# Performance work log

Hardware: AMD Instinct MI355X
Metric: run time of the kernel (lower is better)

## Reference

```python
import jax, jax.numpy as jnp
import numpy as np

N, D, E = 50000, 64, 800000  # nodes, node_dim, edges


def setup_inputs() -> dict:
    key = jax.random.key(0)
    ks = jax.random.split(key, 9)
    def lin(kw, fan_in, fan_out):
        # torch nn.Linear default init: U(-1/sqrt(fan_in), 1/sqrt(fan_in))
        bound = 1.0 / np.sqrt(fan_in)
        kw1, kw2 = jax.random.split(kw)
        W = jax.random.uniform(kw1, (fan_in, fan_out), jnp.float32, -bound, bound)
        b = jax.random.uniform(kw2, (fan_out,), jnp.float32, -bound, bound)
        return W, b
    W1, b1 = lin(ks[0], 2 * D + 2, D)
    W2, b2 = lin(ks[1], D, D // 2)
    W3, b3 = lin(ks[2], D // 2, D // 4)
    return {
        "node_features": jax.random.normal(ks[3], (N, D), jnp.float32),
        "edge_index": jax.random.randint(ks[4], (2, E), 0, N, jnp.int64),
        "spatial_features": jax.random.normal(ks[5], (E, 2), jnp.float32),
        "W1": W1, "b1": b1, "W2": W2, "b2": b2, "W3": W3, "b3": b3,
    }


def reference(node_features, edge_index, spatial_features, W1, b1, W2, b2, W3, b3):
    src = node_features[edge_index[0]]          # [E, D] gather
    dst = node_features[edge_index[1]]          # [E, D] gather
    x = jnp.concatenate([src, dst, spatial_features], axis=1)  # [E, 2D+2]
    h = jax.nn.relu(x @ W1 + b1)                # [E, D]
    h = jax.nn.relu(h @ W2 + b2)                # [E, D//2]
    return h @ W3 + b3                          # [E, D//4]
```

## Files before the change

kernel.cpp:

```cpp
#include <hip/hip_runtime.h>
#include <hip/hip_bf16.h>

#define NE 800000
#define NN 50000
#define TPW 4
#define NTILES (NE / 16)
#define NODE_TILES (NN / 16)
#define W1LD 136

typedef __attribute__((ext_vector_type(8))) short        s16x8;
typedef __attribute__((ext_vector_type(8))) __bf16       bf16x8;
typedef __attribute__((ext_vector_type(4))) float        f32x4;
typedef __attribute__((ext_vector_type(2))) float        f32x2;
typedef __attribute__((ext_vector_type(4))) unsigned int u32x4;
typedef __attribute__((ext_vector_type(2))) unsigned int u32x2;

#define TAB_OFF 16384
#define WS_TAB ((size_t)(TAB_OFF + 2ull * NN * 64) * 2)
#define WS_NFB ((size_t)(TAB_OFF + 1ull * NN * 64) * 2)

__device__ __forceinline__ unsigned short f2bf_bits(float f) {
    __bf16 b = (__bf16)f;
    return __builtin_bit_cast(unsigned short, b);
}

__device__ __forceinline__ unsigned int pkbf(float a, float b) {
    return (unsigned int)f2bf_bits(a) | ((unsigned int)f2bf_bits(b) << 16);
}

__device__ __forceinline__ s16x8 cvt8(f32x4 a, f32x4 b) {
    bf16x8 r;
    r[0] = (__bf16)a[0]; r[1] = (__bf16)a[1]; r[2] = (__bf16)a[2]; r[3] = (__bf16)a[3];
    r[4] = (__bf16)b[0]; r[5] = (__bf16)b[1]; r[6] = (__bf16)b[2]; r[7] = (__bf16)b[3];
    return __builtin_bit_cast(s16x8, r);
}

__global__ __launch_bounds__(256) void node_prep_all(
    const float* __restrict__ nf, const float* __restrict__ W1,
    const float* __restrict__ b1, const float* __restrict__ W2,
    const float* __restrict__ W3, unsigned short* __restrict__ ws) {
    unsigned short* w2t = ws + 10240;
    unsigned short* w3t = ws + 12288;
    unsigned short* At  = ws + TAB_OFF;
    unsigned short* Bt  = At + (size_t)NN * 64;

    __shared__ unsigned short w1l[64 * W1LD];

    const int tid = threadIdx.x, wid = tid >> 6, lane = tid & 63;
    const int lr = lane & 15, lg = lane >> 4;

    for (int i = tid; i < 128 * 64; i += 256) {
        const int k = i >> 6, j = i & 63;
        w1l[j * W1LD + k] = f2bf_bits(W1[i]);
    }
    __syncthreads();

    if (blockIdx.x == 0) {
        for (int i = tid; i < 32 * 64; i += 256) {
            int j = i / 64, k = i % 64;
            w2t[i] = f2bf_bits(W2[k * 32 + j]);
        }
        for (int i = tid; i < 16 * 32; i += 256) {
            int j = i / 32, k = i % 32;
            w3t[i] = f2bf_bits(W3[k * 16 + j]);
        }
    }

    s16x8 w1f[4][4];
    #pragma unroll
    for (int s = 0; s < 4; ++s)
        #pragma unroll
        for (int c = 0; c < 4; ++c)
            w1f[s][c] = *reinterpret_cast<const s16x8*>(
                &w1l[(c * 16 + lr) * W1LD + s * 32 + lg * 8]);

    f32x4 b1q[4];
    #pragma unroll
    for (int c = 0; c < 4; ++c)
        b1q[c] = *reinterpret_cast<const f32x4*>(b1 + c * 16 + lg * 4);

    const int tile = blockIdx.x * 4 + wid;
    if (tile >= NODE_TILES) return;

    const int row = tile * 16 + lr;
    const float* p = nf + (long)row * 64;
    s16x8 nfr[2];
    #pragma unroll
    for (int s = 0; s < 2; ++s) {
        f32x4 a = *reinterpret_cast<const f32x4*>(p + s * 32 + lg * 8);
        f32x4 b = *reinterpret_cast<const f32x4*>(p + s * 32 + lg * 8 + 4);
        nfr[s] = cvt8(a, b);
    }
    f32x4 a4[4], b4[4];
    #pragma unroll
    for (int c = 0; c < 4; ++c) { a4[c] = (f32x4){0,0,0,0}; b4[c] = (f32x4){0,0,0,0}; }
    #pragma unroll
    for (int s = 0; s < 2; ++s)
        #pragma unroll
        for (int c = 0; c < 4; ++c) {
            a4[c] = __builtin_amdgcn_mfma_f32_16x16x32_bf16(w1f[s][c],     nfr[s], a4[c], 0, 0, 0);
            b4[c] = __builtin_amdgcn_mfma_f32_16x16x32_bf16(w1f[s + 2][c], nfr[s], b4[c], 0, 0, 0);
        }
    #pragma unroll
    for (int c = 0; c < 4; ++c) {
        u32x2 pa, pb;
        pa[0] = pkbf(a4[c][0] + b1q[c][0], a4[c][1] + b1q[c][1]);
        pa[1] = pkbf(a4[c][2] + b1q[c][2], a4[c][3] + b1q[c][3]);
        pb[0] = pkbf(b4[c][0], b4[c][1]);
        pb[1] = pkbf(b4[c][2], b4[c][3]);
        *reinterpret_cast<u32x2*>(At + (long)row * 64 + c * 16 + lg * 4) = pa;
        *reinterpret_cast<u32x2*>(Bt + (long)row * 64 + c * 16 + lg * 4) = pb;
    }
}

__device__ __forceinline__ void gatherT(const unsigned short* At, const unsigned short* Bt,
                                        int si, int di, int lg, s16x8 g[4]) {
    const unsigned short* pa = At + (size_t)si * 64 + lg * 8;
    const unsigned short* pb = Bt + (size_t)di * 64 + lg * 8;
    g[0] = *reinterpret_cast<const s16x8*>(pa);
    g[1] = *reinterpret_cast<const s16x8*>(pa + 32);
    g[2] = *reinterpret_cast<const s16x8*>(pb);
    g[3] = *reinterpret_cast<const s16x8*>(pb + 32);
}

__device__ __forceinline__ void compute_tile(
    int tile, const s16x8 cur[4], f32x2 s2,
    const f32x2 c0p[2][4], const f32x2 c1p[2][4],
    const s16x8 w2f[2][2], s16x8 w3f,
    const f32x4 b2v[2], f32x4 b3v,
    unsigned short* h2w, int lg, int lr, float* __restrict__ out) {

    const f32x2 sp0v = {s2[0], s2[0]}, sp1v = {s2[1], s2[1]};

    s16x8 bfr[2];
    #pragma unroll
    for (int jb = 0; jb < 2; ++jb) {
        u32x4 au = __builtin_bit_cast(u32x4, cur[jb]);
        u32x4 bu = __builtin_bit_cast(u32x4, cur[2 + jb]);
        u32x4 pk4;
        #pragma unroll
        for (int q = 0; q < 4; ++q) {
            f32x2 av = {__builtin_bit_cast(float, au[q] << 16),
                        __builtin_bit_cast(float, au[q] & 0xFFFF0000u)};
            f32x2 bv = {__builtin_bit_cast(float, bu[q] << 16),
                        __builtin_bit_cast(float, bu[q] & 0xFFFF0000u)};
            f32x2 h = av + bv;
            h = sp1v * c1p[jb][q] + h;
            h = sp0v * c0p[jb][q] + h;
            pk4[q] = pkbf(fmaxf(h[0], 0.f), fmaxf(h[1], 0.f));
        }
        bfr[jb] = __builtin_bit_cast(s16x8, pk4);
    }

    f32x4 acc2[2];
    #pragma unroll
    for (int c = 0; c < 2; ++c) acc2[c] = (f32x4){0, 0, 0, 0};
    #pragma unroll
    for (int s = 0; s < 2; ++s)
        #pragma unroll
        for (int c = 0; c < 2; ++c)
            acc2[c] = __builtin_amdgcn_mfma_f32_16x16x32_bf16(w2f[s][c], bfr[s], acc2[c], 0, 0, 0);

    #pragma unroll
    for (int c = 0; c < 2; ++c) {
        u32x2 p;
        p[0] = pkbf(fmaxf(acc2[c][0] + b2v[c][0], 0.f), fmaxf(acc2[c][1] + b2v[c][1], 0.f));
        p[1] = pkbf(fmaxf(acc2[c][2] + b2v[c][2], 0.f), fmaxf(acc2[c][3] + b2v[c][3], 0.f));
        *reinterpret_cast<u32x2*>(h2w + c * 16 + lg * 4) = p;
    }

    s16x8 bf3 = *reinterpret_cast<const s16x8*>(h2w + lg * 8);
    f32x4 acc3 = (f32x4){0, 0, 0, 0};
    acc3 = __builtin_amdgcn_mfma_f32_16x16x32_bf16(w3f, bf3, acc3, 0, 0, 0);

    f32x4 o;
    #pragma unroll
    for (int r = 0; r < 4; ++r) o[r] = acc3[r] + b3v[r];
    __builtin_nontemporal_store(o,
        reinterpret_cast<f32x4*>(out + (long)(tile * 16 + lr) * 16 + lg * 4));
}

__global__ __launch_bounds__(256) void edge_mlp_tab(
    const int* __restrict__ ei, const float* __restrict__ sp,
    const float* __restrict__ W1, const float* __restrict__ b2,
    const float* __restrict__ b3, const unsigned short* __restrict__ wsw,
    float* __restrict__ out) {

    const unsigned short* w2t = wsw + 10240;
    const unsigned short* w3t = wsw + 12288;
    const unsigned short* At  = wsw + TAB_OFF;
    const unsigned short* Bt  = At + (size_t)NN * 64;

    __shared__ unsigned short h2s[4 * 16 * 40];

    const int tid = threadIdx.x, wid = tid >> 6, lane = tid & 63;
    const int lr = lane & 15, lg = lane >> 4;

    const int tile0 = (blockIdx.x * 4 + wid) * TPW;

    s16x8 w2f[2][2], w3f;
    #pragma unroll
    for (int s = 0; s < 2; ++s)
        #pragma unroll
        for (int c = 0; c < 2; ++c)
            w2f[s][c] = *reinterpret_cast<const s16x8*>(w2t + (c * 16 + lr) * 64 + s * 32 + lg * 8);
    w3f = *reinterpret_cast<const s16x8*>(w3t + lr * 32 + lg * 8);

    f32x4 b2v[2];
    #pragma unroll
    for (int c = 0; c < 2; ++c) b2v[c] = *reinterpret_cast<const f32x4*>(b2 + c * 16 + lg * 4);
    const f32x4 b3v = *reinterpret_cast<const f32x4*>(b3 + lg * 4);

    f32x2 c0p[2][4], c1p[2][4];
    #pragma unroll
    for (int jb = 0; jb < 2; ++jb) {
        const int j0 = jb * 32 + lg * 8;
        f32x4 x0 = *reinterpret_cast<const f32x4*>(W1 + 128 * 64 + j0);
        f32x4 x1 = *reinterpret_cast<const f32x4*>(W1 + 128 * 64 + j0 + 4);
        f32x4 y0 = *reinterpret_cast<const f32x4*>(W1 + 129 * 64 + j0);
        f32x4 y1 = *reinterpret_cast<const f32x4*>(W1 + 129 * 64 + j0 + 4);
        c0p[jb][0] = (f32x2){x0[0], x0[1]}; c0p[jb][1] = (f32x2){x0[2], x0[3]};
        c0p[jb][2] = (f32x2){x1[0], x1[1]}; c0p[jb][3] = (f32x2){x1[2], x1[3]};
        c1p[jb][0] = (f32x2){y0[0], y0[1]}; c1p[jb][1] = (f32x2){y0[2], y0[3]};
        c1p[jb][2] = (f32x2){y1[0], y1[1]}; c1p[jb][3] = (f32x2){y1[2], y1[3]};
    }

    unsigned short* h2w = h2s + wid * (16 * 40) + lr * 40;

    int si[TPW], di[TPW];
    f32x2 spv[TPW];
    #pragma unroll
    for (int t = 0; t < TPW; ++t) {
        const size_t e = (size_t)(tile0 + t) * 16 + lr;
        si[t] = ei[e];
        di[t] = ei[NE + e];
        spv[t] = *reinterpret_cast<const f32x2*>(sp + 2 * e);
    }

    s16x8 cur[4], nxt[4];
    gatherT(At, Bt, si[0], di[0], lg, cur);

    #pragma unroll
    for (int tt = 0; tt < TPW; ++tt) {
        if (tt + 1 < TPW)
            gatherT(At, Bt, si[tt + 1], di[tt + 1], lg, nxt);
        compute_tile(tile0 + tt, cur, spv[tt], c0p, c1p, w2f, w3f,
                     b2v, b3v, h2w, lg, lr, out);
        #pragma unroll
        for (int s = 0; s < 4; ++s) cur[s] = nxt[s];
    }
}

__global__ void prep(const float* __restrict__ W1, const float* __restrict__ W2,
                     const float* __restrict__ W3, const float* __restrict__ nf,
                     unsigned short* __restrict__ ws, int do_nf) {
    unsigned short* w1t = ws;
    unsigned short* w2t = ws + 10240;
    unsigned short* w3t = ws + 12288;
    int t = blockIdx.x * blockDim.x + threadIdx.x;
    int stride = gridDim.x * blockDim.x;
    for (int i = t; i < 64 * 160; i += stride) {
        int j = i / 160, k = i % 160;
        w1t[i] = f2bf_bits(k < 130 ? W1[k * 64 + j] : 0.0f);
    }
    for (int i = t; i < 32 * 64; i += stride) {
        int j = i / 64, k = i % 64;
        w2t[i] = f2bf_bits(W2[k * 32 + j]);
    }
    for (int i = t; i < 16 * 32; i += stride) {
        int j = i / 32, k = i % 32;
        w3t[i] = f2bf_bits(W3[k * 16 + j]);
    }
    if (do_nf) {
        unsigned short* nfb = ws + TAB_OFF;
        for (int i = t; i < NN * 8; i += stride) {
            f32x4 a = *reinterpret_cast<const f32x4*>(nf + (long)i * 8);
            f32x4 b = *reinterpret_cast<const f32x4*>(nf + (long)i * 8 + 4);
            *reinterpret_cast<s16x8*>(nfb + (long)i * 8) = cvt8(a, b);
        }
    }
}

template <bool BF16NF>
__device__ __forceinline__ void gather4(const unsigned short* nfb, const float* nf,
                                        int si, int di, int lg, s16x8 g[4]) {
    if (BF16NF) {
        #pragma unroll
        for (int s = 0; s < 4; ++s) {
            const int row = (s < 2) ? si : di;
            g[s] = *reinterpret_cast<const s16x8*>(nfb + (long)row * 64 + (s & 1) * 32 + lg * 8);
        }
    } else {
        #pragma unroll
        for (int s = 0; s < 4; ++s) {
            const float* p = nf + (long)((s < 2) ? si : di) * 64 + (s & 1) * 32 + lg * 8;
            f32x4 a = *reinterpret_cast<const f32x4*>(p);
            f32x4 b = *reinterpret_cast<const f32x4*>(p + 4);
            g[s] = cvt8(a, b);
        }
    }
}

template <bool BF16NF>
__global__ __launch_bounds__(256) void edge_mlp_fb(
    const float* __restrict__ nf, const int* __restrict__ ei,
    const float* __restrict__ sp, const float* __restrict__ b1,
    const float* __restrict__ b2, const float* __restrict__ b3,
    const unsigned short* __restrict__ wsw, float* __restrict__ out) {

    const unsigned short* w1t = wsw;
    const unsigned short* w2t = wsw + 10240;
    const unsigned short* w3t = wsw + 12288;
    const unsigned short* nfb = wsw + TAB_OFF;

    __shared__ float h1s[4][16][68];
    __shared__ float h2s[4][16][36];

    const int tid = threadIdx.x, wid = tid >> 6, lane = tid & 63;
    const int lr = lane & 15, lg = lane >> 4;

    s16x8 w1f[5][4], w2f[2][2], w3f;
    #pragma unroll
    for (int s = 0; s < 5; ++s)
        #pragma unroll
        for (int c = 0; c < 4; ++c)
            w1f[s][c] = *reinterpret_cast<const s16x8*>(w1t + (c * 16 + lr) * 160 + s * 32 + lg * 8);
    #pragma unroll
    for (int s = 0; s < 2; ++s)
        #pragma unroll
        for (int c = 0; c < 2; ++c)
            w2f[s][c] = *reinterpret_cast<const s16x8*>(w2t + (c * 16 + lr) * 64 + s * 32 + lg * 8);
    w3f = *reinterpret_cast<const s16x8*>(w3t + lr * 32 + lg * 8);

    float bias1[4], bias2[2], bias3;
    #pragma unroll
    for (int c = 0; c < 4; ++c) bias1[c] = b1[c * 16 + lr];
    #pragma unroll
    for (int c = 0; c < 2; ++c) bias2[c] = b2[c * 16 + lr];
    bias3 = b3[lr];

    const int tile0 = (blockIdx.x * 4 + wid) * 4;
    int si[4], di[4];
    f32x2 spv[4];
    #pragma unroll
    for (int t = 0; t < 4; ++t) {
        const int e = (tile0 + t) * 16 + lr;
        si[t] = ei[e];
        di[t] = ei[NE + e];
        spv[t] = *reinterpret_cast<const f32x2*>(sp + 2 * (size_t)e);
    }

    s16x8 cur[4], nxt[4];
    gather4<BF16NF>(nfb, nf, si[0], di[0], lg, cur);

    #pragma unroll
    for (int tt = 0; tt < 4; ++tt) {
        if (tt + 1 < 4)
            gather4<BF16NF>(nfb, nf, si[tt + 1], di[tt + 1], lg, nxt);

        const int ebase = (tile0 + tt) * 16;

        f32x4 acc1[4];
        #pragma unroll
        for (int c = 0; c < 4; ++c) acc1[c] = (f32x4){0, 0, 0, 0};
        #pragma unroll
        for (int s = 0; s < 4; ++s)
            #pragma unroll
            for (int c = 0; c < 4; ++c)
                acc1[c] = __builtin_amdgcn_mfma_f32_16x16x32_bf16(cur[s], w1f[s][c], acc1[c], 0, 0, 0);
        {
            bf16x8 z;
            #pragma unroll
            for (int j = 0; j < 8; ++j) z[j] = (__bf16)0.0f;
            if (lg == 0) { z[0] = (__bf16)spv[tt][0]; z[1] = (__bf16)spv[tt][1]; }
            s16x8 af = __builtin_bit_cast(s16x8, z);
            #pragma unroll
            for (int c = 0; c < 4; ++c)
                acc1[c] = __builtin_amdgcn_mfma_f32_16x16x32_bf16(af, w1f[4][c], acc1[c], 0, 0, 0);
        }
        #pragma unroll
        for (int c = 0; c < 4; ++c)
            #pragma unroll
            for (int r = 0; r < 4; ++r)
                h1s[wid][lg * 4 + r][c * 16 + lr] = fmaxf(acc1[c][r] + bias1[c], 0.0f);

        f32x4 acc2[2];
        #pragma unroll
        for (int c = 0; c < 2; ++c) acc2[c] = (f32x4){0, 0, 0, 0};
        #pragma unroll
        for (int s = 0; s < 2; ++s) {
            f32x4 a = *reinterpret_cast<const f32x4*>(&h1s[wid][lr][s * 32 + lg * 8]);
            f32x4 b = *reinterpret_cast<const f32x4*>(&h1s[wid][lr][s * 32 + lg * 8 + 4]);
            s16x8 af = cvt8(a, b);
            #pragma unroll
            for (int c = 0; c < 2; ++c)
                acc2[c] = __builtin_amdgcn_mfma_f32_16x16x32_bf16(af, w2f[s][c], acc2[c], 0, 0, 0);
        }
        #pragma unroll
        for (int c = 0; c < 2; ++c)
            #pragma unroll
            for (int r = 0; r < 4; ++r)
                h2s[wid][lg * 4 + r][c * 16 + lr] = fmaxf(acc2[c][r] + bias2[c], 0.0f);

        f32x4 a3 = *reinterpret_cast<const f32x4*>(&h2s[wid][lr][lg * 8]);
        f32x4 b3x = *reinterpret_cast<const f32x4*>(&h2s[wid][lr][lg * 8 + 4]);
        s16x8 af3 = cvt8(a3, b3x);
        f32x4 acc3 = (f32x4){0, 0, 0, 0};
        acc3 = __builtin_amdgcn_mfma_f32_16x16x32_bf16(af3, w3f, acc3, 0, 0, 0);
        #pragma unroll
        for (int r = 0; r < 4; ++r)
            out[(long)(ebase + lg * 4 + r) * 16 + lr] = acc3[r] + bias3;

        #pragma unroll
        for (int s = 0; s < 4; ++s) cur[s] = nxt[s];
    }
}

extern "C" void kernel_launch(void* const* d_in, const int* in_sizes, int n_in,
                              void* d_out, int out_size, void* d_ws, size_t ws_size,
                              hipStream_t stream) {
    const float* nf = (const float*)d_in[0];
    const int*   ei = (const int*)d_in[1];
    const float* sp = (const float*)d_in[2];
    const float* W1 = (const float*)d_in[3];
    const float* b1 = (const float*)d_in[4];
    const float* W2 = (const float*)d_in[5];
    const float* b2 = (const float*)d_in[6];
    const float* W3 = (const float*)d_in[7];
    const float* b3 = (const float*)d_in[8];
    float* out = (float*)d_out;
    unsigned short* wsw = (unsigned short*)d_ws;

    const bool tab  = (ws_size >= WS_TAB);
    const bool bnfb = (!tab && ws_size >= WS_NFB);

    if (tab) {
        const int pblocks = (NODE_TILES + 3) / 4;
        hipLaunchKernelGGL(node_prep_all, dim3(pblocks), dim3(256), 0, stream,
                           nf, W1, b1, W2, W3, wsw);
        const int blocks = NTILES / TPW / 4;
        hipLaunchKernelGGL(edge_mlp_tab, dim3(blocks), dim3(256), 0, stream,
                           ei, sp, W1, b2, b3, wsw, out);
    } else {
        hipLaunchKernelGGL(prep, dim3(64), dim3(256), 0, stream,
                           W1, W2, W3, nf, wsw, bnfb ? 1 : 0);
        const int blocks = NTILES / 4 / 4;
        if (bnfb)
            hipLaunchKernelGGL(edge_mlp_fb<true>, dim3(blocks), dim3(256), 0, stream,
                               nf, ei, sp, b1, b2, b3, wsw, out);
        else
            hipLaunchKernelGGL(edge_mlp_fb<false>, dim3(blocks), dim3(256), 0, stream,
                               nf, ei, sp, b1, b2, b3, wsw, out);
    }
}
```

Measured before the change: 60.23 us.

## Split W1 packing into single-block kernel and halve edge tiles per wave

Moves the bf16 conversion and fragment packing of W1, W2 and W3 out of the per-block node prep kernel into a separate one-block kernel that writes MFMA-ready fragments to workspace. Each node_prep block then loads its W1 fragments directly from global memory, so the 782 blocks no longer each convert and transpose the whole W1 through shared memory. TPW also drops from 4 to 2, doubling the edge kernel's grid for more parallelism. The cost is an extra kernel launch plus serialization behind a single-block kernel.

```diff
diff --git a/kernel.cpp b/kernel.cpp
--- a/kernel.cpp
+++ b/kernel.cpp
@@ -3,10 +3,9 @@
 
 #define NE 800000
 #define NN 50000
-#define TPW 4
+#define TPW 2
 #define NTILES (NE / 16)
 #define NODE_TILES (NN / 16)
-#define W1LD 136
 
 typedef __attribute__((ext_vector_type(8))) short        s16x8;
 typedef __attribute__((ext_vector_type(8))) __bf16       bf16x8;
@@ -35,44 +34,45 @@
     return __builtin_bit_cast(s16x8, r);
 }
 
-__global__ __launch_bounds__(256) void node_prep_all(
-    const float* __restrict__ nf, const float* __restrict__ W1,
-    const float* __restrict__ b1, const float* __restrict__ W2,
+__global__ __launch_bounds__(256) void pack_weights_tab(
+    const float* __restrict__ W1, const float* __restrict__ W2,
     const float* __restrict__ W3, unsigned short* __restrict__ ws) {
+    __shared__ unsigned short w1l[128 * 64];
+    const int tid = threadIdx.x;
+    for (int i = tid; i < 128 * 64; i += 256) w1l[i] = f2bf_bits(W1[i]);
+    __syncthreads();
+    for (int i = tid; i < 8192; i += 256) {
+        const int b = i & 7, idx = i >> 3;
+        const int f = idx & 15, lane = idx >> 4;
+        const int s = f >> 2, c = f & 3, lr = lane & 15, lg = lane >> 4;
+        ws[i] = w1l[(s * 32 + lg * 8 + b) * 64 + c * 16 + lr];
+    }
     unsigned short* w2t = ws + 10240;
     unsigned short* w3t = ws + 12288;
-    unsigned short* At  = ws + TAB_OFF;
-    unsigned short* Bt  = At + (size_t)NN * 64;
-
-    __shared__ unsigned short w1l[64 * W1LD];
-
+    for (int i = tid; i < 32 * 64; i += 256) {
+        int j = i / 64, k = i % 64;
+        w2t[i] = f2bf_bits(W2[k * 32 + j]);
+    }
+    for (int i = tid; i < 16 * 32; i += 256) {
+        int j = i / 32, k = i % 32;
+        w3t[i] = f2bf_bits(W3[k * 16 + j]);
+    }
+}
+
+__global__ __launch_bounds__(256) void node_prep(
+    const float* __restrict__ nf, const float* __restrict__ b1,
+    const unsigned short* __restrict__ wsw, unsigned short* __restrict__ At,
+    unsigned short* __restrict__ Bt) {
     const int tid = threadIdx.x, wid = tid >> 6, lane = tid & 63;
     const int lr = lane & 15, lg = lane >> 4;
 
-    for (int i = tid; i < 128 * 64; i += 256) {
-        const int k = i >> 6, j = i & 63;
-        w1l[j * W1LD + k] = f2bf_bits(W1[i]);
-    }
-    __syncthreads();
-
-    if (blockIdx.x == 0) {
-        for (int i = tid; i < 32 * 64; i += 256) {
-            int j = i / 64, k = i % 64;
-            w2t[i] = f2bf_bits(W2[k * 32 + j]);
-        }
-        for (int i = tid; i < 16 * 32; i += 256) {
-            int j = i / 32, k = i % 32;
-            w3t[i] = f2bf_bits(W3[k * 16 + j]);
-        }
-    }
-
     s16x8 w1f[4][4];
     #pragma unroll
     for (int s = 0; s < 4; ++s)
         #pragma unroll
         for (int c = 0; c < 4; ++c)
             w1f[s][c] = *reinterpret_cast<const s16x8*>(
-                &w1l[(c * 16 + lr) * W1LD + s * 32 + lg * 8]);
+                wsw + ((size_t)lane * 16 + s * 4 + c) * 8);
 
     f32x4 b1q[4];
     #pragma unroll
@@ -435,9 +435,11 @@
     const bool bnfb = (!tab && ws_size >= WS_NFB);
 
     if (tab) {
+        hipLaunchKernelGGL(pack_weights_tab, dim3(1), dim3(256), 0, stream,
+                           W1, W2, W3, wsw);
         const int pblocks = (NODE_TILES + 3) / 4;
-        hipLaunchKernelGGL(node_prep_all, dim3(pblocks), dim3(256), 0, stream,
-                           nf, W1, b1, W2, W3, wsw);
+        hipLaunchKernelGGL(node_prep, dim3(pblocks), dim3(256), 0, stream,
+                           nf, b1, wsw, wsw + TAB_OFF, wsw + TAB_OFF + (size_t)NN * 64);
         const int blocks = NTILES / TPW / 4;
         hipLaunchKernelGGL(edge_mlp_tab, dim3(blocks), dim3(256), 0, stream,
                            ei, sp, W1, b2, b3, wsw, out);
```

Result: slower. 78.44 us (+30.2%).

## Fuse node prep and edge MLP into one persistent cooperative kernel

Applied to the files above, without the earlier changes.

Replaces the two-launch path (node table precompute, then edge MLP) with a single persistent cooperative kernel. Its waves first build the per-node W1 projection tables, then pass a grid-wide sync and loop over edge tile pairs while prefetching the next indices. This removes one kernel launch and the gap between kernels. In exchange it adds a grid barrier, host-side occupancy queries on every call, and weight fragments built from strided global reads. If the cooperative launch fails, it falls back to the old two-kernel path.

```diff
diff --git a/kernel.cpp b/kernel.cpp
--- a/kernel.cpp
+++ b/kernel.cpp
@@ -1,11 +1,15 @@
 #include <hip/hip_runtime.h>
 #include <hip/hip_bf16.h>
+#include <hip/hip_cooperative_groups.h>
+
+namespace cg = cooperative_groups;
 
 #define NE 800000
 #define NN 50000
 #define TPW 4
 #define NTILES (NE / 16)
 #define NODE_TILES (NN / 16)
+#define NUNITS (NTILES / 2)
 #define W1LD 136
 
 typedef __attribute__((ext_vector_type(8))) short        s16x8;
@@ -33,84 +37,6 @@
     r[0] = (__bf16)a[0]; r[1] = (__bf16)a[1]; r[2] = (__bf16)a[2]; r[3] = (__bf16)a[3];
     r[4] = (__bf16)b[0]; r[5] = (__bf16)b[1]; r[6] = (__bf16)b[2]; r[7] = (__bf16)b[3];
     return __builtin_bit_cast(s16x8, r);
-}
-
-__global__ __launch_bounds__(256) void node_prep_all(
-    const float* __restrict__ nf, const float* __restrict__ W1,
-    const float* __restrict__ b1, const float* __restrict__ W2,
-    const float* __restrict__ W3, unsigned short* __restrict__ ws) {
-    unsigned short* w2t = ws + 10240;
-    unsigned short* w3t = ws + 12288;
-    unsigned short* At  = ws + TAB_OFF;
-    unsigned short* Bt  = At + (size_t)NN * 64;
-
-    __shared__ unsigned short w1l[64 * W1LD];
-
-    const int tid = threadIdx.x, wid = tid >> 6, lane = tid & 63;
-    const int lr = lane & 15, lg = lane >> 4;
-
-    for (int i = tid; i < 128 * 64; i += 256) {
-        const int k = i >> 6, j = i & 63;
-        w1l[j * W1LD + k] = f2bf_bits(W1[i]);
-    }
-    __syncthreads();
-
-    if (blockIdx.x == 0) {
-        for (int i = tid; i < 32 * 64; i += 256) {
-            int j = i / 64, k = i % 64;
-            w2t[i] = f2bf_bits(W2[k * 32 + j]);
-        }
-        for (int i = tid; i < 16 * 32; i += 256) {
-            int j = i / 32, k = i % 32;
-            w3t[i] = f2bf_bits(W3[k * 16 + j]);
-        }
-    }
-
-    s16x8 w1f[4][4];
-    #pragma unroll
-    for (int s = 0; s < 4; ++s)
-        #pragma unroll
-        for (int c = 0; c < 4; ++c)
-            w1f[s][c] = *reinterpret_cast<const s16x8*>(
-                &w1l[(c * 16 + lr) * W1LD + s * 32 + lg * 8]);
-
-    f32x4 b1q[4];
-    #pragma unroll
-    for (int c = 0; c < 4; ++c)
-        b1q[c] = *reinterpret_cast<const f32x4*>(b1 + c * 16 + lg * 4);
-
-    const int tile = blockIdx.x * 4 + wid;
-    if (tile >= NODE_TILES) return;
-
-    const int row = tile * 16 + lr;
-    const float* p = nf + (long)row * 64;
-    s16x8 nfr[2];
-    #pragma unroll
-    for (int s = 0; s < 2; ++s) {
-        f32x4 a = *reinterpret_cast<const f32x4*>(p + s * 32 + lg * 8);
-        f32x4 b = *reinterpret_cast<const f32x4*>(p + s * 32 + lg * 8 + 4);
-        nfr[s] = cvt8(a, b);
-    }
-    f32x4 a4[4], b4[4];
-    #pragma unroll
-    for (int c = 0; c < 4; ++c) { a4[c] = (f32x4){0,0,0,0}; b4[c] = (f32x4){0,0,0,0}; }
-    #pragma unroll
-    for (int s = 0; s < 2; ++s)
-        #pragma unroll
-        for (int c = 0; c < 4; ++c) {
-            a4[c] = __builtin_amdgcn_mfma_f32_16x16x32_bf16(w1f[s][c],     nfr[s], a4[c], 0, 0, 0);
-            b4[c] = __builtin_amdgcn_mfma_f32_16x16x32_bf16(w1f[s + 2][c], nfr[s], b4[c], 0, 0, 0);
-        }
-    #pragma unroll
-    for (int c = 0; c < 4; ++c) {
-        u32x2 pa, pb;
-        pa[0] = pkbf(a4[c][0] + b1q[c][0], a4[c][1] + b1q[c][1]);
-        pa[1] = pkbf(a4[c][2] + b1q[c][2], a4[c][3] + b1q[c][3]);
-        pb[0] = pkbf(b4[c][0], b4[c][1]);
-        pb[1] = pkbf(b4[c][2], b4[c][3]);
-        *reinterpret_cast<u32x2*>(At + (long)row * 64 + c * 16 + lg * 4) = pa;
-        *reinterpret_cast<u32x2*>(Bt + (long)row * 64 + c * 16 + lg * 4) = pb;
-    }
 }
 
 __device__ __forceinline__ void gatherT(const unsigned short* At, const unsigned short* Bt,
@@ -178,6 +104,231 @@
     for (int r = 0; r < 4; ++r) o[r] = acc3[r] + b3v[r];
     __builtin_nontemporal_store(o,
         reinterpret_cast<f32x4*>(out + (long)(tile * 16 + lr) * 16 + lg * 4));
+}
+
+__device__ __forceinline__ void load_unit_idx(const int* __restrict__ ei,
+                                              const float* __restrict__ sp, int u, int lr,
+                                              int si[2], int di[2], f32x2 spv[2]) {
+    #pragma unroll
+    for (int v = 0; v < 2; ++v) {
+        const size_t e = (size_t)(u * 2 + v) * 16 + lr;
+        si[v] = ei[e];
+        di[v] = ei[NE + e];
+        spv[v] = *reinterpret_cast<const f32x2*>(sp + 2 * e);
+    }
+}
+
+__global__ __launch_bounds__(256, 4) void fused_all(
+    const float* __restrict__ nf, const int* __restrict__ ei,
+    const float* __restrict__ sp, const float* __restrict__ W1,
+    const float* __restrict__ b1, const float* __restrict__ W2,
+    const float* __restrict__ b2, const float* __restrict__ W3,
+    const float* __restrict__ b3, unsigned short* __restrict__ tab,
+    float* __restrict__ out) {
+
+    unsigned short* At = tab;
+    unsigned short* Bt = tab + (size_t)NN * 64;
+
+    __shared__ unsigned short h2s[4 * 16 * 40];
+
+    const int tid = threadIdx.x, wid = tid >> 6, lane = tid & 63;
+    const int lr = lane & 15, lg = lane >> 4;
+    const int gwave  = blockIdx.x * 4 + wid;
+    const int nwaves = gridDim.x * 4;
+
+    if (gwave < NODE_TILES) {
+        s16x8 w1f[4][4];
+        #pragma unroll
+        for (int s = 0; s < 4; ++s)
+            #pragma unroll
+            for (int c = 0; c < 4; ++c) {
+                bf16x8 w;
+                #pragma unroll
+                for (int b = 0; b < 8; ++b)
+                    w[b] = (__bf16)W1[(s * 32 + lg * 8 + b) * 64 + c * 16 + lr];
+                w1f[s][c] = __builtin_bit_cast(s16x8, w);
+            }
+        f32x4 b1q[4];
+        #pragma unroll
+        for (int c = 0; c < 4; ++c)
+            b1q[c] = *reinterpret_cast<const f32x4*>(b1 + c * 16 + lg * 4);
+
+        for (int tile = gwave; tile < NODE_TILES; tile += nwaves) {
+            const int row = tile * 16 + lr;
+            const float* p = nf + (long)row * 64;
+            s16x8 nfr[2];
+            #pragma unroll
+            for (int s = 0; s < 2; ++s) {
+                f32x4 a = *reinterpret_cast<const f32x4*>(p + s * 32 + lg * 8);
+                f32x4 b = *reinterpret_cast<const f32x4*>(p + s * 32 + lg * 8 + 4);
+                nfr[s] = cvt8(a, b);
+            }
+            f32x4 a4[4], b4[4];
+            #pragma unroll
+            for (int c = 0; c < 4; ++c) { a4[c] = (f32x4){0,0,0,0}; b4[c] = (f32x4){0,0,0,0}; }
+            #pragma unroll
+            for (int s = 0; s < 2; ++s)
+                #pragma unroll
+                for (int c = 0; c < 4; ++c) {
+                    a4[c] = __builtin_amdgcn_mfma_f32_16x16x32_bf16(w1f[s][c],     nfr[s], a4[c], 0, 0, 0);
+                    b4[c] = __builtin_amdgcn_mfma_f32_16x16x32_bf16(w1f[s + 2][c], nfr[s], b4[c], 0, 0, 0);
+                }
+            #pragma unroll
+            for (int c = 0; c < 4; ++c) {
+                u32x2 pa, pb;
+                pa[0] = pkbf(a4[c][0] + b1q[c][0], a4[c][1] + b1q[c][1]);
+                pa[1] = pkbf(a4[c][2] + b1q[c][2], a4[c][3] + b1q[c][3]);
+                pb[0] = pkbf(b4[c][0], b4[c][1]);
+                pb[1] = pkbf(b4[c][2], b4[c][3]);
+                *reinterpret_cast<u32x2*>(At + (long)row * 64 + c * 16 + lg * 4) = pa;
+                *reinterpret_cast<u32x2*>(Bt + (long)row * 64 + c * 16 + lg * 4) = pb;
+            }
+        }
+    }
+
+    __threadfence();
+    cg::this_grid().sync();
+
+    s16x8 w2f[2][2];
+    #pragma unroll
+    for (int s = 0; s < 2; ++s)
+        #pragma unroll
+        for (int c = 0; c < 2; ++c) {
+            bf16x8 w;
+            #pragma unroll
+            for (int b = 0; b < 8; ++b)
+                w[b] = (__bf16)W2[(s * 32 + lg * 8 + b) * 32 + c * 16 + lr];
+            w2f[s][c] = __builtin_bit_cast(s16x8, w);
+        }
+    s16x8 w3f;
+    {
+        bf16x8 w;
+        #pragma unroll
+        for (int b = 0; b < 8; ++b) w[b] = (__bf16)W3[(lg * 8 + b) * 16 + lr];
+        w3f = __builtin_bit_cast(s16x8, w);
+    }
+
+    f32x4 b2v[2];
+    #pragma unroll
+    for (int c = 0; c < 2; ++c) b2v[c] = *reinterpret_cast<const f32x4*>(b2 + c * 16 + lg * 4);
+    const f32x4 b3v = *reinterpret_cast<const f32x4*>(b3 + lg * 4);
+
+    f32x2 c0p[2][4], c1p[2][4];
+    #pragma unroll
+    for (int jb = 0; jb < 2; ++jb) {
+        const int j0 = jb * 32 + lg * 8;
+        f32x4 x0 = *reinterpret_cast<const f32x4*>(W1 + 128 * 64 + j0);
+        f32x4 x1 = *reinterpret_cast<const f32x4*>(W1 + 128 * 64 + j0 + 4);
+        f32x4 y0 = *reinterpret_cast<const f32x4*>(W1 + 129 * 64 + j0);
+        f32x4 y1 = *reinterpret_cast<const f32x4*>(W1 + 129 * 64 + j0 + 4);
+        c0p[jb][0] = (f32x2){x0[0], x0[1]}; c0p[jb][1] = (f32x2){x0[2], x0[3]};
+        c0p[jb][2] = (f32x2){x1[0], x1[1]}; c0p[jb][3] = (f32x2){x1[2], x1[3]};
+        c1p[jb][0] = (f32x2){y0[0], y0[1]}; c1p[jb][1] = (f32x2){y0[2], y0[3]};
+        c1p[jb][2] = (f32x2){y1[0], y1[1]}; c1p[jb][3] = (f32x2){y1[2], y1[3]};
+    }
+
+    unsigned short* h2w = h2s + wid * (16 * 40) + lr * 40;
+
+    int u = gwave;
+    if (u < NUNITS) {
+        int si[2], di[2];
+        f32x2 spv[2];
+        load_unit_idx(ei, sp, u, lr, si, di, spv);
+        for (;;) {
+            const int un = u + nwaves;
+            const bool more = (un < NUNITS);
+            s16x8 cur[4], nxt[4];
+            gatherT(At, Bt, si[0], di[0], lg, cur);
+            int si2[2], di2[2];
+            f32x2 spv2[2];
+            if (more) load_unit_idx(ei, sp, un, lr, si2, di2, spv2);
+            gatherT(At, Bt, si[1], di[1], lg, nxt);
+            compute_tile(u * 2,     cur, spv[0], c0p, c1p, w2f, w3f, b2v, b3v, h2w, lg, lr, out);
+            compute_tile(u * 2 + 1, nxt, spv[1], c0p, c1p, w2f, w3f, b2v, b3v, h2w, lg, lr, out);
+            if (!more) break;
+            #pragma unroll
+            for (int v = 0; v < 2; ++v) { si[v] = si2[v]; di[v] = di2[v]; spv[v] = spv2[v]; }
+            u = un;
+        }
+    }
+}
+
+__global__ __launch_bounds__(256) void node_prep_all(
+    const float* __restrict__ nf, const float* __restrict__ W1,
+    const float* __restrict__ b1, const float* __restrict__ W2,
+    const float* __restrict__ W3, unsigned short* __restrict__ ws) {
+    unsigned short* w2t = ws + 10240;
+    unsigned short* w3t = ws + 12288;
+    unsigned short* At  = ws + TAB_OFF;
+    unsigned short* Bt  = At + (size_t)NN * 64;
+
+    __shared__ unsigned short w1l[64 * W1LD];
+
+    const int tid = threadIdx.x, wid = tid >> 6, lane = tid & 63;
+    const int lr = lane & 15, lg = lane >> 4;
+
+    for (int i = tid; i < 128 * 64; i += 256) {
+        const int k = i >> 6, j = i & 63;
+        w1l[j * W1LD + k] = f2bf_bits(W1[i]);
+    }
+    __syncthreads();
+
+    if (blockIdx.x == 0) {
+        for (int i = tid; i < 32 * 64; i += 256) {
+            int j = i / 64, k = i % 64;
+            w2t[i] = f2bf_bits(W2[k * 32 + j]);
+        }
+        for (int i = tid; i < 16 * 32; i += 256) {
+            int j = i / 32, k = i % 32;
+            w3t[i] = f2bf_bits(W3[k * 16 + j]);
+        }
+    }
+
+    s16x8 w1f[4][4];
+    #pragma unroll
+    for (int s = 0; s < 4; ++s)
+        #pragma unroll
+        for (int c = 0; c < 4; ++c)
+            w1f[s][c] = *reinterpret_cast<const s16x8*>(
+                &w1l[(c * 16 + lr) * W1LD + s * 32 + lg * 8]);
+
+    f32x4 b1q[4];
+    #pragma unroll
+    for (int c = 0; c < 4; ++c)
+        b1q[c] = *reinterpret_cast<const f32x4*>(b1 + c * 16 + lg * 4);
+
+    const int tile = blockIdx.x * 4 + wid;
+    if (tile >= NODE_TILES) return;
+
+    const int row = tile * 16 + lr;
+    const float* p = nf + (long)row * 64;
+    s16x8 nfr[2];
+    #pragma unroll
+    for (int s = 0; s < 2; ++s) {
+        f32x4 a = *reinterpret_cast<const f32x4*>(p + s * 32 + lg * 8);
+        f32x4 b = *reinterpret_cast<const f32x4*>(p + s * 32 + lg * 8 + 4);
+        nfr[s] = cvt8(a, b);
+    }
+    f32x4 a4[4], b4[4];
+    #pragma unroll
+    for (int c = 0; c < 4; ++c) { a4[c] = (f32x4){0,0,0,0}; b4[c] = (f32x4){0,0,0,0}; }
+    #pragma unroll
+    for (int s = 0; s < 2; ++s)
+        #pragma unroll
+        for (int c = 0; c < 4; ++c) {
+            a4[c] = __builtin_amdgcn_mfma_f32_16x16x32_bf16(w1f[s][c],     nfr[s], a4[c], 0, 0, 0);
+            b4[c] = __builtin_amdgcn_mfma_f32_16x16x32_bf16(w1f[s + 2][c], nfr[s], b4[c], 0, 0, 0);
+        }
+    #pragma unroll
+    for (int c = 0; c < 4; ++c) {
+        u32x2 pa, pb;
+        pa[0] = pkbf(a4[c][0] + b1q[c][0], a4[c][1] + b1q[c][1]);
+        pa[1] = pkbf(a4[c][2] + b1q[c][2], a4[c][3] + b1q[c][3]);
+        pb[0] = pkbf(b4[c][0], b4[c][1]);
+        pb[1] = pkbf(b4[c][2], b4[c][3]);
+        *reinterpret_cast<u32x2*>(At + (long)row * 64 + c * 16 + lg * 4) = pa;
+        *reinterpret_cast<u32x2*>(Bt + (long)row * 64 + c * 16 + lg * 4) = pb;
+    }
 }
 
 __global__ __launch_bounds__(256) void edge_mlp_tab(
@@ -435,12 +586,30 @@
     const bool bnfb = (!tab && ws_size >= WS_NFB);
 
     if (tab) {
-        const int pblocks = (NODE_TILES + 3) / 4;
-        hipLaunchKernelGGL(node_prep_all, dim3(pblocks), dim3(256), 0, stream,
-                           nf, W1, b1, W2, W3, wsw);
-        const int blocks = NTILES / TPW / 4;
-        hipLaunchKernelGGL(edge_mlp_tab, dim3(blocks), dim3(256), 0, stream,
-                           ei, sp, W1, b2, b3, wsw, out);
+        bool done = false;
+        int maxb = 0, ncu = 0;
+        if (hipOccupancyMaxActiveBlocksPerMultiprocessor(
+                &maxb, (const void*)fused_all, 256, 0) == hipSuccess &&
+            hipDeviceGetAttribute(&ncu, hipDeviceAttributeMultiprocessorCount, 0)
+                == hipSuccess && maxb > 0 && ncu > 0) {
+            int grid = maxb * ncu;
+            if (grid > 2048) grid = 2048;
+            unsigned short* tabp = wsw + TAB_OFF;
+            void* args[] = {(void*)&nf, (void*)&ei, (void*)&sp, (void*)&W1,
+                            (void*)&b1, (void*)&W2, (void*)&b2, (void*)&W3,
+                            (void*)&b3, (void*)&tabp, (void*)&out};
+            hipError_t le = hipLaunchCooperativeKernel(
+                (const void*)fused_all, dim3(grid), dim3(256), args, 0, stream);
+            done = (le == hipSuccess);
+        }
+        if (!done) {
+            const int pblocks = (NODE_TILES + 3) / 4;
+            hipLaunchKernelGGL(node_prep_all, dim3(pblocks), dim3(256), 0, stream,
+                               nf, W1, b1, W2, W3, wsw);
+            const int blocks = NTILES / TPW / 4;
+            hipLaunchKernelGGL(edge_mlp_tab, dim3(blocks), dim3(256), 0, stream,
+                               ei, sp, W1, b2, b3, wsw, out);
+        }
     } else {
         hipLaunchKernelGGL(prep, dim3(64), dim3(256), 0, stream,
                            W1, W2, W3, nf, wsw, bnfb ? 1 : 0);
```

After: 179.0 us. +197.1%, slower.

## Deepen gather prefetch to two tiles ahead and swizzle W1 LDS layout

Applied to the files above, without the earlier changes.

Each wave in the edge kernel now processes five tiles instead of four. It keeps three gather buffers so table gathers run two tiles ahead of compute, aiming to hide more of the latency of random node-table reads. The node-prep kernel now loads W1 with float4 vector loads and stores it into LDS with an XOR swizzle, meant to reduce bank conflicts on both the write and the fragment reads. The costs are higher register pressure from the extra buffer and fewer, larger blocks. NTILES/(TPW*4) divides evenly at 2500 blocks, so no edges are dropped.

```diff
diff --git a/kernel.cpp b/kernel.cpp
--- a/kernel.cpp
+++ b/kernel.cpp
@@ -3,13 +3,15 @@
 
 #define NE 800000
 #define NN 50000
-#define TPW 4
+#define TPW 5
 #define NTILES (NE / 16)
 #define NODE_TILES (NN / 16)
-#define W1LD 136
+#define W1STR 136
 
 typedef __attribute__((ext_vector_type(8))) short        s16x8;
+typedef __attribute__((ext_vector_type(4))) short        s16x4;
 typedef __attribute__((ext_vector_type(8))) __bf16       bf16x8;
+typedef __attribute__((ext_vector_type(4))) __bf16       bf16x4;
 typedef __attribute__((ext_vector_type(4))) float        f32x4;
 typedef __attribute__((ext_vector_type(2))) float        f32x2;
 typedef __attribute__((ext_vector_type(4))) unsigned int u32x4;
@@ -33,6 +35,10 @@
     r[0] = (__bf16)a[0]; r[1] = (__bf16)a[1]; r[2] = (__bf16)a[2]; r[3] = (__bf16)a[3];
     r[4] = (__bf16)b[0]; r[5] = (__bf16)b[1]; r[6] = (__bf16)b[2]; r[7] = (__bf16)b[3];
     return __builtin_bit_cast(s16x8, r);
+}
+
+__device__ __forceinline__ int w1addr(int k, int j) {
+    return j * W1STR + (((k >> 3) ^ ((j >> 2) & 15)) << 3) + (k & 7);
 }
 
 __global__ __launch_bounds__(256) void node_prep_all(
@@ -44,14 +50,19 @@
     unsigned short* At  = ws + TAB_OFF;
     unsigned short* Bt  = At + (size_t)NN * 64;
 
-    __shared__ unsigned short w1l[64 * W1LD];
+    __shared__ unsigned short w1l[64 * W1STR];
 
     const int tid = threadIdx.x, wid = tid >> 6, lane = tid & 63;
     const int lr = lane & 15, lg = lane >> 4;
 
-    for (int i = tid; i < 128 * 64; i += 256) {
-        const int k = i >> 6, j = i & 63;
-        w1l[j * W1LD + k] = f2bf_bits(W1[i]);
+    #pragma unroll
+    for (int it = 0; it < 8; ++it) {
+        const int i = it * 1024 + tid * 4;
+        const int k = i >> 6, j0 = i & 63;
+        f32x4 v = *reinterpret_cast<const f32x4*>(W1 + i);
+        #pragma unroll
+        for (int q = 0; q < 4; ++q)
+            w1l[w1addr(k, j0 + q)] = f2bf_bits(v[q]);
     }
     __syncthreads();
 
@@ -72,7 +83,7 @@
         #pragma unroll
         for (int c = 0; c < 4; ++c)
             w1f[s][c] = *reinterpret_cast<const s16x8*>(
-                &w1l[(c * 16 + lr) * W1LD + s * 32 + lg * 8]);
+                &w1l[w1addr(s * 32 + lg * 8, c * 16 + lr)]);
 
     f32x4 b1q[4];
     #pragma unroll
@@ -237,18 +248,21 @@
         spv[t] = *reinterpret_cast<const f32x2*>(sp + 2 * e);
     }
 
-    s16x8 cur[4], nxt[4];
-    gatherT(At, Bt, si[0], di[0], lg, cur);
-
-    #pragma unroll
-    for (int tt = 0; tt < TPW; ++tt) {
-        if (tt + 1 < TPW)
-            gatherT(At, Bt, si[tt + 1], di[tt + 1], lg, nxt);
-        compute_tile(tile0 + tt, cur, spv[tt], c0p, c1p, w2f, w3f,
-                     b2v, b3v, h2w, lg, lr, out);
-        #pragma unroll
-        for (int s = 0; s < 4; ++s) cur[s] = nxt[s];
-    }
+    s16x8 gA[4], gB[4], gC[4];
+    gatherT(At, Bt, si[0], di[0], lg, gA);
+    gatherT(At, Bt, si[1], di[1], lg, gB);
+
+    gatherT(At, Bt, si[2], di[2], lg, gC);
+    compute_tile(tile0 + 0, gA, spv[0], c0p, c1p, w2f, w3f, b2v, b3v, h2w, lg, lr, out);
+
+    gatherT(At, Bt, si[3], di[3], lg, gA);
+    compute_tile(tile0 + 1, gB, spv[1], c0p, c1p, w2f, w3f, b2v, b3v, h2w, lg, lr, out);
+
+    gatherT(At, Bt, si[4], di[4], lg, gB);
+    compute_tile(tile0 + 2, gC, spv[2], c0p, c1p, w2f, w3f, b2v, b3v, h2w, lg, lr, out);
+
+    compute_tile(tile0 + 3, gA, spv[3], c0p, c1p, w2f, w3f, b2v, b3v, h2w, lg, lr, out);
+    compute_tile(tile0 + 4, gB, spv[4], c0p, c1p, w2f, w3f, b2v, b3v, h2w, lg, lr, out);
 }
 
 __global__ void prep(const float* __restrict__ W1, const float* __restrict__ W2,
@@ -438,7 +452,7 @@
         const int pblocks = (NODE_TILES + 3) / 4;
         hipLaunchKernelGGL(node_prep_all, dim3(pblocks), dim3(256), 0, stream,
                            nf, W1, b1, W2, W3, wsw);
-        const int blocks = NTILES / TPW / 4;
+        const int blocks = NTILES / (TPW * 4);
         hipLaunchKernelGGL(edge_mlp_tab, dim3(blocks), dim3(256), 0, stream,
                            ei, sp, W1, b2, b3, wsw, out);
     } else {
```

Result: faster. 57.08 us (-5.2%).
